# Kernel optimization log

Measured on AMD Instinct MI355X. Metric: run time of the kernel, lower is better.

The kernel has to match this reference:

```python
import jax, jax.numpy as jnp
import numpy as np

NCH, P, T, BS = 129, 4, 64000, 8
FRM_RATE, TC, HAIR_TC, SHFT, FAC = 16, 8.0, 0.5, 0, 1.0
L_FRM = FRM_RATE * (2 ** (4 + SHFT))            # 256 samples per frame
ALPHA = float(np.exp(-1.0 / (TC * 2 ** (4 + SHFT))))       # temporal integrator pole
BETA = float(np.exp(-1.0 / (HAIR_TC * 2 ** (4 + SHFT))))   # hair-cell LPF pole


def setup_inputs() -> dict:
    rng = np.random.default_rng(0)
    # stable order-4 cochlear IIRs: 2 conjugate pole pairs inside unit circle
    r = rng.uniform(0.8, 0.97, (NCH, P // 2))
    th = rng.uniform(0.05, np.pi - 0.05, (NCH, P // 2))
    A = np.stack([
        np.poly(np.concatenate([r[c] * np.exp(1j * th[c]), r[c] * np.exp(-1j * th[c])])).real
        for c in range(NCH)
    ]).astype(np.float32)                        # [NCH, P+1], A[:,0]==1
    B = (rng.standard_normal((NCH, P + 1)) * 0.1).astype(np.float32)
    key = jax.random.key(0)
    wav = jax.random.normal(key, (BS, T), dtype=jnp.float32)
    return {"wavData": wav, "coch_B": jnp.asarray(B), "coch_A": jnp.asarray(A)}


def iir_lfilter(b, a, x):
    # b, a: [nCh, P+1] (a[:,0] == 1), x: [bs, T] -> y: [nCh, bs, T]
    # direct-form II transposed, all channels in one scan over time
    bt = b[:, None, :]                           # [nCh, 1, P+1]
    at = a[:, None, :]
    z0 = jnp.zeros((b.shape[0], x.shape[0], b.shape[1] - 1), x.dtype)

    def step(z, xt):                             # z: [nCh, bs, P], xt: [bs]
        y = bt[..., 0] * xt[None, :] + z[..., 0]
        z_shift = jnp.concatenate([z[..., 1:], jnp.zeros_like(z[..., :1])], -1)
        z = z_shift + bt[..., 1:] * xt[None, :, None] - at[..., 1:] * y[..., None]
        return z, y

    _, y = jax.lax.scan(step, z0, x.T)           # y: [T, nCh, bs]
    return jnp.moveaxis(y, 0, -1)                # [nCh, bs, T]


def first_order_iir(x, c):
    # y[t] = x[t] + c * y[t-1] along the last axis (lfilter b=[1,0], a=[1,-c])
    def combine(e1, e2):
        a1, b1 = e1
        a2, b2 = e2
        return a1 * a2, b1 * a2 + b2

    coef = jnp.full_like(x, jnp.asarray(c, x.dtype))
    _, y = jax.lax.associative_scan(combine, (coef, x), axis=-1)
    return y


def reference(wavData, coch_B, coch_A):
    y1 = iir_lfilter(coch_B, coch_A, wavData)        # cochlear filterbank [nCh, bs, T]
    y2 = jax.nn.sigmoid(FAC * y1)                    # hair-cell nonlinearity
    y2 = first_order_iir(y2, BETA)                   # hair-cell membrane LPF
    y2_prev = jnp.concatenate([y2[:1], y2[:-1]], 0)  # previous channel (ch 0 diffs itself -> 0)
    y4 = jnp.maximum(y2 - y2_prev, 0.0)              # lateral inhibition + half-wave rectify
    y5 = first_order_iir(y4, ALPHA)                  # temporal integration (alpha != 0 branch)
    aud = y5[..., 0:T - 1:L_FRM]                     # frame-rate downsample [nCh, bs, nFrm]
    return jnp.transpose(aud, (1, 0, 2))             # [bs, nCh, nFrm]
```

## Files before the change

### kernel.cpp

```cpp
#include <hip/hip_runtime.h>
#include <math.h>

#define NCH 129
#define BS 8
#define TLEN 64000
#define CHUNK 256
#define WARM 64
#define NH 250
#define TILE 256
#define LFRM 256
#define NFRM 250
#define NSEQ (NCH * BS)
#define NBK (BS * NFRM)
#define NT (BS * NH)
#define KA_EDGE 16
#define KC_EDGE 8
#define KC_MAIN (NBK / 4)
#define SEG 25
#define LSEG 10
#define SGRP 17

#define SEQ4(h, b, c) ((size_t)(h) * NSEQ + (size_t)(b) * NCH + (c))

typedef float f2 __attribute__((ext_vector_type(2)));

__device__ __forceinline__ f2 mk2(float a, float b) { f2 r; r.x = a; r.y = b; return r; }

__device__ __forceinline__ f2 fma2(f2 a, f2 b, f2 c) {
#if __has_builtin(__builtin_elementwise_fma)
    return __builtin_elementwise_fma(a, b, c);
#else
    f2 r; r.x = fmaf(a.x, b.x, c.x); r.y = fmaf(a.y, b.y, c.y); return r;
#endif
}

__device__ __forceinline__ f2 sig2(f2 v) {
    f2 r;
    r.x = __builtin_amdgcn_rcpf(1.0f + __expf(-v.x));
    r.y = __builtin_amdgcn_rcpf(1.0f + __expf(-v.y));
    return r;
}

struct C2 { f2 b0, b1, b2, b3, b4, a1, a2, a3, a4; };

__device__ __forceinline__ C2 load_coef2(const float* __restrict__ B,
                                         const float* __restrict__ A,
                                         int cx, int cy) {
    C2 q;
    q.b0 = mk2(B[cx * 5 + 0], B[cy * 5 + 0]);
    q.b1 = mk2(B[cx * 5 + 1], B[cy * 5 + 1]);
    q.b2 = mk2(B[cx * 5 + 2], B[cy * 5 + 2]);
    q.b3 = mk2(B[cx * 5 + 3], B[cy * 5 + 3]);
    q.b4 = mk2(B[cx * 5 + 4], B[cy * 5 + 4]);
    q.a1 = mk2(A[cx * 5 + 1], A[cy * 5 + 1]);
    q.a2 = mk2(A[cx * 5 + 2], A[cy * 5 + 2]);
    q.a3 = mk2(A[cx * 5 + 3], A[cy * 5 + 3]);
    q.a4 = mk2(A[cx * 5 + 4], A[cy * 5 + 4]);
    return q;
}

__device__ __forceinline__ f2 iir2_step(const C2& q, float x,
                                        f2& z0, f2& z1, f2& z2, f2& z3) {
    f2 xx = mk2(x, x);
    f2 y = fma2(q.b0, xx, z0);
    z0 = fma2(-q.a1, y, fma2(q.b1, xx, z1));
    z1 = fma2(-q.a2, y, fma2(q.b2, xx, z2));
    z2 = fma2(-q.a3, y, fma2(q.b3, xx, z3));
    z3 = fma2(-q.a4, y, q.b4 * xx);
    return y;
}

struct Coef { float b0, b1, b2, b3, b4, a1, a2, a3, a4; };
__device__ __forceinline__ Coef load_coef(const float* __restrict__ B,
                                          const float* __restrict__ A, int c) {
    Coef q;
    q.b0 = B[c * 5 + 0]; q.b1 = B[c * 5 + 1]; q.b2 = B[c * 5 + 2];
    q.b3 = B[c * 5 + 3]; q.b4 = B[c * 5 + 4];
    q.a1 = A[c * 5 + 1]; q.a2 = A[c * 5 + 2];
    q.a3 = A[c * 5 + 3]; q.a4 = A[c * 5 + 4];
    return q;
}
__device__ __forceinline__ float iir_step(const Coef& q, float x,
                                          float& z0, float& z1, float& z2, float& z3) {
    float y = fmaf(q.b0, x, z0);
    z0 = fmaf(-q.a1, y, fmaf(q.b1, x, z1));
    z1 = fmaf(-q.a2, y, fmaf(q.b2, x, z2));
    z2 = fmaf(-q.a3, y, fmaf(q.b3, x, z3));
    z3 = fmaf(-q.a4, y, q.b4 * x);
    return y;
}

#define WSTEP(xv)                                                              \
    { f2 y_ = iir2_step(q, (xv), z0, z1, z2, z3);                              \
      u = fma2(beta2, u, sig2(y_)); }
#define MSTEP(xv)                                                              \
    { f2 y_ = iir2_step(q, (xv), z0, z1, z2, z3);                              \
      u = fma2(beta2, u, sig2(y_));                                            \
      float un_ = __shfl_down(u.x, 1, 64);                                     \
      float y4o_ = fmaxf(u.y - u.x, 0.0f);                                     \
      float y4e_ = fmaxf(pend_un - pend_ub, 0.0f);                             \
      g2 = fma2(alpha2, g2, mk2(y4o_, y4e_));                                  \
      pend_un = un_; pend_ub = u.y; }

#define MDECL(X) float X##00, X##01, X##02, X##03, X##10, X##11, X##12, X##13, \
                       X##20, X##21, X##22, X##23, X##30, X##31, X##32, X##33
#define MCOPY(D, S) D##00=S##00; D##01=S##01; D##02=S##02; D##03=S##03;        \
                    D##10=S##10; D##11=S##11; D##12=S##12; D##13=S##13;        \
                    D##20=S##20; D##21=S##21; D##22=S##22; D##23=S##23;        \
                    D##30=S##30; D##31=S##31; D##32=S##32; D##33=S##33
#define MROW(R, X, Y, i)                                                       \
    R##i##0 = fmaf(X##i##0, Y##00, fmaf(X##i##1, Y##10, fmaf(X##i##2, Y##20, X##i##3 * Y##30))); \
    R##i##1 = fmaf(X##i##0, Y##01, fmaf(X##i##1, Y##11, fmaf(X##i##2, Y##21, X##i##3 * Y##31))); \
    R##i##2 = fmaf(X##i##0, Y##02, fmaf(X##i##1, Y##12, fmaf(X##i##2, Y##22, X##i##3 * Y##32))); \
    R##i##3 = fmaf(X##i##0, Y##03, fmaf(X##i##1, Y##13, fmaf(X##i##2, Y##23, X##i##3 * Y##33)))
#define MMUL(R, X, Y) MROW(R, X, Y, 0); MROW(R, X, Y, 1); MROW(R, X, Y, 2); MROW(R, X, Y, 3)
#define MV(r, X, v)                                                            \
    r.x = fmaf(X##00, v.x, fmaf(X##01, v.y, fmaf(X##02, v.z, X##03 * v.w)));   \
    r.y = fmaf(X##10, v.x, fmaf(X##11, v.y, fmaf(X##12, v.z, X##13 * v.w)));   \
    r.z = fmaf(X##20, v.x, fmaf(X##21, v.y, fmaf(X##22, v.z, X##23 * v.w)));   \
    r.w = fmaf(X##30, v.x, fmaf(X##31, v.y, fmaf(X##32, v.z, X##33 * v.w)))
#define BUILD_MPOW(M1, a1, a2, a3, a4, NSQ)                                    \
    M1##00 = -(a1); M1##01 = 1.f; M1##02 = 0.f; M1##03 = 0.f;                  \
    M1##10 = -(a2); M1##11 = 0.f; M1##12 = 1.f; M1##13 = 0.f;                  \
    M1##20 = -(a3); M1##21 = 0.f; M1##22 = 0.f; M1##23 = 1.f;                  \
    M1##30 = -(a4); M1##31 = 0.f; M1##32 = 0.f; M1##33 = 0.f;                  \
    for (int s_ = 0; s_ < (NSQ); ++s_) { MDECL(T_); MMUL(T_, M1, M1); MCOPY(M1, T_); }

#define AFF_STEP(M, e, d)                                                      \
    {   float4 t_; MV(t_, M, e);                                               \
        e.x = t_.x + d.x; e.y = t_.y + d.y;                                    \
        e.z = t_.z + d.z; e.w = t_.w + d.w; }

__global__ __launch_bounds__(128, 8) void kA_forced_state(
        const float* __restrict__ wav, const float* __restrict__ B,
        const float* __restrict__ A, float* __restrict__ D,
        float* __restrict__ W) {
    __shared__ float xs[CHUNK];
    int blk = blockIdx.x;
    if (blk < KA_EDGE) {
        int item = blk * 128 + threadIdx.x;
        if (item >= NT) return;
        int b = item / NH;
        int h = item - b * NH;
        const float* xg = wav + (size_t)b * TLEN + (size_t)h * CHUNK;
        Coef q = load_coef(B, A, 128);
        float z0 = 0.f, z1 = 0.f, z2 = 0.f, z3 = 0.f;
        #pragma unroll 4
        for (int j = 0; j < CHUNK - WARM; ++j) {
            (void)iir_step(q, xg[j], z0, z1, z2, z3);
        }
        ((float4*)W)[SEQ4(h, b, 128)] = make_float4(z0, z1, z2, z3);
        #pragma unroll 4
        for (int j = CHUNK - WARM; j < CHUNK; ++j) {
            (void)iir_step(q, xg[j], z0, z1, z2, z3);
        }
        ((float4*)D)[SEQ4(h, b, 128)] = make_float4(z0, z1, z2, z3);
        return;
    }
    int mblk = blk - KA_EDGE;
    int b = mblk / NH;
    int h = mblk - b * NH;
    const float* xg = wav + (size_t)b * TLEN + (size_t)h * CHUNK;
    xs[threadIdx.x] = xg[threadIdx.x];
    xs[threadIdx.x + 128] = xg[threadIdx.x + 128];
    __syncthreads();
    int c = threadIdx.x;
    Coef q = load_coef(B, A, c);
    float z0 = 0.f, z1 = 0.f, z2 = 0.f, z3 = 0.f;
    #pragma unroll 8
    for (int j = 0; j < CHUNK - WARM; ++j) {
        (void)iir_step(q, xs[j], z0, z1, z2, z3);
    }
    ((float4*)W)[SEQ4(h, b, c)] = make_float4(z0, z1, z2, z3);
    #pragma unroll 8
    for (int j = CHUNK - WARM; j < CHUNK; ++j) {
        (void)iir_step(q, xs[j], z0, z1, z2, z3);
    }
    ((float4*)D)[SEQ4(h, b, c)] = make_float4(z0, z1, z2, z3);
}

__global__ __launch_bounds__(64) void kB1_fold(
        const float* __restrict__ A, const float* __restrict__ D,
        float* __restrict__ E) {
    int seg = blockIdx.x / SGRP;
    int s = (blockIdx.x % SGRP) * 64 + threadIdx.x;
    if (s >= NSEQ) return;
    int c = s % NCH;
    float a1 = A[c * 5 + 1], a2 = A[c * 5 + 2], a3 = A[c * 5 + 3], a4 = A[c * 5 + 4];
    MDECL(M1); BUILD_MPOW(M1, a1, a2, a3, a4, 8);
    const float4* db = (const float4*)D;
    float4 e = make_float4(0.f, 0.f, 0.f, 0.f);
    size_t base = (size_t)seg * LSEG * NSEQ + s;
    #pragma unroll
    for (int i = 0; i < LSEG; ++i) {
        float4 d = db[base + (size_t)i * NSEQ];
        AFF_STEP(M1, e, d);
    }
    ((float4*)E)[(size_t)seg * NSEQ + s] = e;
}

__global__ __launch_bounds__(64) void kB2_carry(
        const float* __restrict__ A, float* __restrict__ E) {
    int s = blockIdx.x * 64 + threadIdx.x;
    if (s >= NSEQ) return;
    int c = s % NCH;
    float a1 = A[c * 5 + 1], a2 = A[c * 5 + 2], a3 = A[c * 5 + 3], a4 = A[c * 5 + 4];
    MDECL(M1); BUILD_MPOW(M1, a1, a2, a3, a4, 8);
    MDECL(P2); MMUL(P2, M1, M1);
    MDECL(P4); MMUL(P4, P2, P2);
    MDECL(P8); MMUL(P8, P4, P4);
    MDECL(ML); MMUL(ML, P8, P2);
    float4* E4 = (float4*)E;
    float4 Z = make_float4(0.f, 0.f, 0.f, 0.f);
    float4 Eseg = E4[s];
    for (int seg = 0; seg < SEG; ++seg) {
        float4 Enext;
        if (seg + 1 < SEG) Enext = E4[(size_t)(seg + 1) * NSEQ + s];
        else               Enext = Z;
        E4[(size_t)seg * NSEQ + s] = Z;
        AFF_STEP(ML, Z, Eseg);
        Eseg = Enext;
    }
}

__global__ __launch_bounds__(64) void kB3_replay(
        const float* __restrict__ A, const float* __restrict__ D,
        const float* __restrict__ W, float* __restrict__ ZW,
        const float* __restrict__ E) {
    int seg = blockIdx.x / SGRP;
    int s = (blockIdx.x % SGRP) * 64 + threadIdx.x;
    if (s >= NSEQ) return;
    int c = s % NCH;
    float a1 = A[c * 5 + 1], a2 = A[c * 5 + 2], a3 = A[c * 5 + 3], a4 = A[c * 5 + 4];
    MDECL(M64); BUILD_MPOW(M64, a1, a2, a3, a4, 6);
    MDECL(M128); MMUL(M128, M64, M64);
    MDECL(M192); MMUL(M192, M128, M64);
    MDECL(M256); MMUL(M256, M128, M128);
    const float4* db = (const float4*)D;
    const float4* wb = (const float4*)W;
    float4* zwb = (float4*)ZW;
    float4 z = ((const float4*)E)[(size_t)seg * NSEQ + s];
    int h0 = seg * LSEG;
    #pragma unroll
    for (int i = 0; i < LSEG; ++i) {
        size_t ix = (size_t)(h0 + i) * NSEQ + s;
        float4 d = db[ix];
        float4 w = wb[ix];
        float4 zw; MV(zw, M192, z);
        zw.x += w.x; zw.y += w.y; zw.z += w.z; zw.w += w.w;
        zwb[ix] = zw;
        AFF_STEP(M256, z, d);
    }
}

__global__ __launch_bounds__(256, 8) void kC_main(
        const float* __restrict__ wav, const float* __restrict__ B,
        const float* __restrict__ A, const float* __restrict__ ZW,
        float* __restrict__ G, float* __restrict__ y4f,
        float beta, float alpha) {
    __shared__ float4 xs4[4 * 80];
    int blk = blockIdx.x;
    const f2 beta2 = mk2(beta, beta);
    const f2 alpha2 = mk2(alpha, alpha);

    if (blk < KC_EDGE) {
        int item = blk * 256 + threadIdx.x;
        if (item >= NBK) return;
        int b = item / NFRM;
        int r = item - b * NFRM;
        C2 q = load_coef2(B, A, 127, 128);
        f2 z0 = mk2(0.f, 0.f), z1 = z0, z2 = z0, z3 = z0, u = z0;
        const float* xg;
        if (r > 0) {
            float4 vx = ((const float4*)ZW)[SEQ4(r - 1, b, 127)];
            float4 vy = ((const float4*)ZW)[SEQ4(r - 1, b, 128)];
            z0 = mk2(vx.x, vy.x); z1 = mk2(vx.y, vy.y);
            z2 = mk2(vx.z, vy.z); z3 = mk2(vx.w, vy.w);
            xg = wav + (size_t)b * TLEN + (size_t)r * TILE - WARM;
            #pragma unroll 2
            for (int j = 0; j < WARM; ++j) WSTEP(xg[j]);
            xg += WARM;
        } else {
            xg = wav + (size_t)b * TLEN;
        }
        float g4 = 0.f, yfirst = 0.f;
        #pragma unroll 2
        for (int j = 0; j < TILE; ++j) {
            f2 y_ = iir2_step(q, xg[j], z0, z1, z2, z3);
            u = fma2(beta2, u, sig2(y_));
            float y4 = fmaxf(u.y - u.x, 0.0f);
            if (j == 0) yfirst = y4;
            g4 = fmaf(alpha, g4, y4);
        }
        size_t idx = ((size_t)b * NFRM + r) * NCH + 128;
        G[idx] = g4;
        y4f[idx] = yfirst;
        return;
    }

    int wave = threadIdx.x >> 6;
    int t = threadIdx.x & 63;
    int tile = (blk - KC_EDGE) * 4 + wave;
    int b = tile / NFRM;
    int r = tile - b * NFRM;
    int n4 = (r > 0) ? 80 : 64;
    const float* xg = wav + (size_t)b * TLEN +
                      ((r > 0) ? (size_t)r * TILE - WARM : (size_t)0);
    float4* seg = xs4 + wave * 80;
    for (int i = t; i < n4; i += 64) seg[i] = ((const float4*)xg)[i];
    __syncthreads();

    int cA = 2 * t, cB = 2 * t + 1;
    C2 q = load_coef2(B, A, cA, cB);
    f2 z0 = mk2(0.f, 0.f), z1 = z0, z2 = z0, z3 = z0, u = z0;
    int gbase = 0;
    if (r > 0) {
        float4 vx = ((const float4*)ZW)[SEQ4(r - 1, b, cA)];
        float4 vy = ((const float4*)ZW)[SEQ4(r - 1, b, cB)];
        z0 = mk2(vx.x, vy.x); z1 = mk2(vx.y, vy.y);
        z2 = mk2(vx.z, vy.z); z3 = mk2(vx.w, vy.w);
        for (int g = 0; g < WARM / 4; ++g) {
            float4 xq = seg[g];
            WSTEP(xq.x); WSTEP(xq.y); WSTEP(xq.z); WSTEP(xq.w);
        }
        gbase = WARM / 4;
    }

    f2 g2;
    float fo, fe, pend_un, pend_ub;
    {
        float4 xq = seg[gbase];
        f2 y_ = iir2_step(q, xq.x, z0, z1, z2, z3);
        u = fma2(beta2, u, sig2(y_));
        float un_ = __shfl_down(u.x, 1, 64);
        float y4o_ = fmaxf(u.y - u.x, 0.0f);
        fo = y4o_;
        g2 = mk2(y4o_, 0.0f);
        pend_un = un_; pend_ub = u.y;
        y_ = iir2_step(q, xq.y, z0, z1, z2, z3);
        u = fma2(beta2, u, sig2(y_));
        un_ = __shfl_down(u.x, 1, 64);
        y4o_ = fmaxf(u.y - u.x, 0.0f);
        float y4e_ = fmaxf(pend_un - pend_ub, 0.0f);
        fe = y4e_;
        g2 = fma2(alpha2, g2, mk2(y4o_, y4e_));
        pend_un = un_; pend_ub = u.y;
        MSTEP(xq.z); MSTEP(xq.w);
    }
    for (int g = gbase + 1; g < gbase + TILE / 4; ++g) {
        float4 xq = seg[g];
        MSTEP(xq.x); MSTEP(xq.y); MSTEP(xq.z); MSTEP(xq.w);
    }
    float y4e_last = fmaxf(pend_un - pend_ub, 0.0f);
    float go = g2.x;
    float ge = fmaf(alpha, g2.y, y4e_last);

    size_t base = ((size_t)b * NFRM + r) * NCH;
    G[base + cB] = go;
    y4f[base + cB] = fo;
    if (t < 63) {
        G[base + cB + 1] = ge;
        y4f[base + cB + 1] = fe;
    }
}

#define KD_LOAD(gn, yn, i)                                                     \
    {   int kk = k0 + (i); int kcl = (kk < NFRM) ? kk : (NFRM - 1);            \
        size_t ix = ((size_t)b * NFRM + kcl) * NCH + c;                        \
        gn = G[ix]; yn = y4f[ix];                                              \
        if (kk >= NFRM) { gn = 0.f; yn = 0.f; } }
#define KD_REPLAY(gn, yn, i)                                                   \
    {   int kk = k0 + (i);                                                     \
        if (kk < NFRM) o[kk] = fmaf(alpha, sv, yn);                            \
        sv = fmaf(aL, sv, gn); }

__global__ __launch_bounds__(256) void kD_scan_par(
        const float* __restrict__ G, const float* __restrict__ y4f,
        float* __restrict__ out, float alpha, float aL) {
    int id = blockIdx.x * 4 + (threadIdx.x >> 6);
    int lane = threadIdx.x & 63;
    if (id >= NSEQ) return;
    int b = id / NCH;
    int c = id - b * NCH;
    float* o = out + (size_t)id * NFRM;
    int k0 = lane * 4;
    if (c == 0) {
        #pragma unroll
        for (int i = 0; i < 4; ++i) {
            int kk = k0 + i;
            if (kk < NFRM) o[kk] = 0.0f;
        }
        return;
    }
    float g0, g1, g2v, g3, y0, y1, y2v, y3;
    KD_LOAD(g0, y0, 0); KD_LOAD(g1, y1, 1); KD_LOAD(g2v, y2v, 2); KD_LOAD(g3, y3, 3);
    float e = g0;
    e = fmaf(aL, e, g1);
    e = fmaf(aL, e, g2v);
    e = fmaf(aL, e, g3);
    float aL2 = aL * aL;
    float f = aL2 * aL2;
    for (int s = 0; s < 6; ++s) {
        int off = 1 << s;
        float src = __shfl_up(e, off, 64);
        if (lane < off) src = 0.f;
        e = fmaf(f, src, e);
        f = f * f;
    }
    float sv = __shfl_up(e, 1, 64);
    if (lane == 0) sv = 0.f;
    KD_REPLAY(g0, y0, 0); KD_REPLAY(g1, y1, 1);
    KD_REPLAY(g2v, y2v, 2); KD_REPLAY(g3, y3, 3);
}

extern "C" void kernel_launch(void* const* d_in, const int* in_sizes, int n_in,
                              void* d_out, int out_size, void* d_ws, size_t ws_size,
                              hipStream_t stream) {
    const float* wav = (const float*)d_in[0];
    const float* Bc  = (const float*)d_in[1];
    const float* Ac  = (const float*)d_in[2];
    float* out = (float*)d_out;

    float* D   = (float*)d_ws;
    float* W   = D + (size_t)NH * NSEQ * 4;
    float* ZW  = W + (size_t)NH * NSEQ * 4;
    float* G   = ZW + (size_t)NH * NSEQ * 4;
    float* y4f = G + (size_t)NBK * NCH;
    float* E   = y4f + (size_t)NBK * NCH;

    const float alpha  = (float)exp(-1.0 / 128.0);
    const float beta   = (float)exp(-1.0 / 8.0);
    const float alphaL = (float)exp(-256.0 / 128.0);

    kA_forced_state<<<KA_EDGE + NT, 128, 0, stream>>>(wav, Bc, Ac, D, W);
    kB1_fold<<<SEG * SGRP, 64, 0, stream>>>(Ac, D, E);
    kB2_carry<<<SGRP, 64, 0, stream>>>(Ac, E);
    kB3_replay<<<SEG * SGRP, 64, 0, stream>>>(Ac, D, W, ZW, E);
    kC_main<<<KC_EDGE + KC_MAIN, 256, 0, stream>>>(wav, Bc, Ac, ZW, G, y4f, beta, alpha);
    kD_scan_par<<<NSEQ / 4, 256, 0, stream>>>(G, y4f, out, alpha, alphaL);
}
```

Before: 132.6 us.

## Pack two channels per thread in forced-state kernel with packed FMA

The forced-state kernel now runs one 64-lane wave per time tile, with each lane handling two channels through packed v_pk_fma_f32 via inline asm. The block grows to 256 threads covering four tiles, and each wave loads its input into LDS as float4. Negated A coefficients are precomputed so the packed FMAs need no negation, which also affects the other users of iir2_step. The aim is to halve the per-channel instruction count and widen blocks, at the cost of fewer threads in flight and inline asm that blocks compiler scheduling.

```diff
diff --git a/kernel.cpp b/kernel.cpp
--- a/kernel.cpp
+++ b/kernel.cpp
@@ -13,7 +13,8 @@
 #define NSEQ (NCH * BS)
 #define NBK (BS * NFRM)
 #define NT (BS * NH)
-#define KA_EDGE 16
+#define KA_EDGE 8
+#define KA_MAIN (NT / 4)
 #define KC_EDGE 8
 #define KC_MAIN (NBK / 4)
 #define SEG 25
@@ -27,11 +28,14 @@
 __device__ __forceinline__ f2 mk2(float a, float b) { f2 r; r.x = a; r.y = b; return r; }
 
 __device__ __forceinline__ f2 fma2(f2 a, f2 b, f2 c) {
-#if __has_builtin(__builtin_elementwise_fma)
-    return __builtin_elementwise_fma(a, b, c);
-#else
-    f2 r; r.x = fmaf(a.x, b.x, c.x); r.y = fmaf(a.y, b.y, c.y); return r;
-#endif
+    f2 d;
+    asm("v_pk_fma_f32 %0, %1, %2, %3" : "=v"(d) : "v"(a), "v"(b), "v"(c));
+    return d;
+}
+__device__ __forceinline__ f2 mul2(f2 a, f2 b) {
+    f2 d;
+    asm("v_pk_mul_f32 %0, %1, %2" : "=v"(d) : "v"(a), "v"(b));
+    return d;
 }
 
 __device__ __forceinline__ f2 sig2(f2 v) {
@@ -41,7 +45,7 @@
     return r;
 }
 
-struct C2 { f2 b0, b1, b2, b3, b4, a1, a2, a3, a4; };
+struct C2 { f2 b0, b1, b2, b3, b4, na1, na2, na3, na4; };
 
 __device__ __forceinline__ C2 load_coef2(const float* __restrict__ B,
                                          const float* __restrict__ A,
@@ -52,10 +56,10 @@
     q.b2 = mk2(B[cx * 5 + 2], B[cy * 5 + 2]);
     q.b3 = mk2(B[cx * 5 + 3], B[cy * 5 + 3]);
     q.b4 = mk2(B[cx * 5 + 4], B[cy * 5 + 4]);
-    q.a1 = mk2(A[cx * 5 + 1], A[cy * 5 + 1]);
-    q.a2 = mk2(A[cx * 5 + 2], A[cy * 5 + 2]);
-    q.a3 = mk2(A[cx * 5 + 3], A[cy * 5 + 3]);
-    q.a4 = mk2(A[cx * 5 + 4], A[cy * 5 + 4]);
+    q.na1 = mk2(-A[cx * 5 + 1], -A[cy * 5 + 1]);
+    q.na2 = mk2(-A[cx * 5 + 2], -A[cy * 5 + 2]);
+    q.na3 = mk2(-A[cx * 5 + 3], -A[cy * 5 + 3]);
+    q.na4 = mk2(-A[cx * 5 + 4], -A[cy * 5 + 4]);
     return q;
 }
 
@@ -63,10 +67,10 @@
                                         f2& z0, f2& z1, f2& z2, f2& z3) {
     f2 xx = mk2(x, x);
     f2 y = fma2(q.b0, xx, z0);
-    z0 = fma2(-q.a1, y, fma2(q.b1, xx, z1));
-    z1 = fma2(-q.a2, y, fma2(q.b2, xx, z2));
-    z2 = fma2(-q.a3, y, fma2(q.b3, xx, z3));
-    z3 = fma2(-q.a4, y, q.b4 * xx);
+    z0 = fma2(q.na1, y, fma2(q.b1, xx, z1));
+    z1 = fma2(q.na2, y, fma2(q.b2, xx, z2));
+    z2 = fma2(q.na3, y, fma2(q.b3, xx, z3));
+    z3 = fma2(q.na4, y, mul2(q.b4, xx));
     return y;
 }
 
@@ -90,6 +94,7 @@
     return y;
 }
 
+#define ISTEP(xv) { (void)iir2_step(q, (xv), z0, z1, z2, z3); }
 #define WSTEP(xv)                                                              \
     { f2 y_ = iir2_step(q, (xv), z0, z1, z2, z3);                              \
       u = fma2(beta2, u, sig2(y_)); }
@@ -131,14 +136,14 @@
         e.x = t_.x + d.x; e.y = t_.y + d.y;                                    \
         e.z = t_.z + d.z; e.w = t_.w + d.w; }
 
-__global__ __launch_bounds__(128, 8) void kA_forced_state(
+__global__ __launch_bounds__(256, 8) void kA_forced_state(
         const float* __restrict__ wav, const float* __restrict__ B,
         const float* __restrict__ A, float* __restrict__ D,
         float* __restrict__ W) {
-    __shared__ float xs[CHUNK];
+    __shared__ float4 xs4[4 * 64];
     int blk = blockIdx.x;
     if (blk < KA_EDGE) {
-        int item = blk * 128 + threadIdx.x;
+        int item = blk * 256 + threadIdx.x;
         if (item >= NT) return;
         int b = item / NH;
         int h = item - b * NH;
@@ -157,26 +162,31 @@
         ((float4*)D)[SEQ4(h, b, 128)] = make_float4(z0, z1, z2, z3);
         return;
     }
-    int mblk = blk - KA_EDGE;
-    int b = mblk / NH;
-    int h = mblk - b * NH;
+    int wave = threadIdx.x >> 6;
+    int t = threadIdx.x & 63;
+    int tile = (blk - KA_EDGE) * 4 + wave;
+    int b = tile / NH;
+    int h = tile - b * NH;
     const float* xg = wav + (size_t)b * TLEN + (size_t)h * CHUNK;
-    xs[threadIdx.x] = xg[threadIdx.x];
-    xs[threadIdx.x + 128] = xg[threadIdx.x + 128];
+    float4* seg = xs4 + wave * 64;
+    seg[t] = ((const float4*)xg)[t];
     __syncthreads();
-    int c = threadIdx.x;
-    Coef q = load_coef(B, A, c);
-    float z0 = 0.f, z1 = 0.f, z2 = 0.f, z3 = 0.f;
-    #pragma unroll 8
-    for (int j = 0; j < CHUNK - WARM; ++j) {
-        (void)iir_step(q, xs[j], z0, z1, z2, z3);
-    }
-    ((float4*)W)[SEQ4(h, b, c)] = make_float4(z0, z1, z2, z3);
-    #pragma unroll 8
-    for (int j = CHUNK - WARM; j < CHUNK; ++j) {
-        (void)iir_step(q, xs[j], z0, z1, z2, z3);
-    }
-    ((float4*)D)[SEQ4(h, b, c)] = make_float4(z0, z1, z2, z3);
+
+    int cA = 2 * t, cB = 2 * t + 1;
+    C2 q = load_coef2(B, A, cA, cB);
+    f2 z0 = mk2(0.f, 0.f), z1 = z0, z2 = z0, z3 = z0;
+    for (int g = 0; g < (CHUNK - WARM) / 4; ++g) {
+        float4 xq = seg[g];
+        ISTEP(xq.x); ISTEP(xq.y); ISTEP(xq.z); ISTEP(xq.w);
+    }
+    ((float4*)W)[SEQ4(h, b, cA)] = make_float4(z0.x, z1.x, z2.x, z3.x);
+    ((float4*)W)[SEQ4(h, b, cB)] = make_float4(z0.y, z1.y, z2.y, z3.y);
+    for (int g = (CHUNK - WARM) / 4; g < CHUNK / 4; ++g) {
+        float4 xq = seg[g];
+        ISTEP(xq.x); ISTEP(xq.y); ISTEP(xq.z); ISTEP(xq.w);
+    }
+    ((float4*)D)[SEQ4(h, b, cA)] = make_float4(z0.x, z1.x, z2.x, z3.x);
+    ((float4*)D)[SEQ4(h, b, cB)] = make_float4(z0.y, z1.y, z2.y, z3.y);
 }
 
 __global__ __launch_bounds__(64) void kB1_fold(
@@ -432,7 +442,7 @@
     const float beta   = (float)exp(-1.0 / 8.0);
     const float alphaL = (float)exp(-256.0 / 128.0);
 
-    kA_forced_state<<<KA_EDGE + NT, 128, 0, stream>>>(wav, Bc, Ac, D, W);
+    kA_forced_state<<<KA_EDGE + KA_MAIN, 256, 0, stream>>>(wav, Bc, Ac, D, W);
     kB1_fold<<<SEG * SGRP, 64, 0, stream>>>(Ac, D, E);
     kB2_carry<<<SGRP, 64, 0, stream>>>(Ac, E);
     kB3_replay<<<SEG * SGRP, 64, 0, stream>>>(Ac, D, W, ZW, E);
```

New measurement: 131.6 us. Within noise of the previous version (-0.7%).

## Remap main kernels to one channel per lane with split channel halves

Applied to the files above, without the earlier changes.

The main path of kC now gives each lane a single channel. Channels 0-63 and 64-127 run in separate waves, replacing the old scheme where each lane handled two adjacent channels with packed float2 math. Lateral inhibition uses a scalar shfl_up. The wave boundary pairs (63,64) and (127,128) move to edge blocks. kA is regrouped into 256-thread blocks that each cover two tiles and load input with float4. The change roughly doubles the lane count and shortens each lane's dependent chain, at the cost of losing packed-FMA throughput and adding extra edge work.

```diff
diff --git a/kernel.cpp b/kernel.cpp
--- a/kernel.cpp
+++ b/kernel.cpp
@@ -8,14 +8,14 @@
 #define WARM 64
 #define NH 250
 #define TILE 256
-#define LFRM 256
 #define NFRM 250
 #define NSEQ (NCH * BS)
 #define NBK (BS * NFRM)
 #define NT (BS * NH)
-#define KA_EDGE 16
-#define KC_EDGE 8
-#define KC_MAIN (NBK / 4)
+#define KA_EDGE 8
+#define KA_MAIN (NT / 2)
+#define KC_EDGE 16
+#define KC_MAIN (NBK / 2)
 #define SEG 25
 #define LSEG 10
 #define SGRP 17
@@ -34,11 +34,11 @@
 #endif
 }
 
+__device__ __forceinline__ float sigf(float v) {
+    return __builtin_amdgcn_rcpf(1.0f + __expf(-v));
+}
 __device__ __forceinline__ f2 sig2(f2 v) {
-    f2 r;
-    r.x = __builtin_amdgcn_rcpf(1.0f + __expf(-v.x));
-    r.y = __builtin_amdgcn_rcpf(1.0f + __expf(-v.y));
-    return r;
+    f2 r; r.x = sigf(v.x); r.y = sigf(v.y); return r;
 }
 
 struct C2 { f2 b0, b1, b2, b3, b4, a1, a2, a3, a4; };
@@ -90,17 +90,20 @@
     return y;
 }
 
+#define SISTEP(xv) { (void)iir_step(q, (xv), z0, z1, z2, z3); }
+#define SWSTEP(xv)                                                             \
+    { float y_ = iir_step(q, (xv), z0, z1, z2, z3);                            \
+      u = fmaf(beta, u, sigf(y_)); }
+#define SSTEP(xv)                                                              \
+    { float y_ = iir_step(q, (xv), z0, z1, z2, z3);                            \
+      u = fmaf(beta, u, sigf(y_));                                             \
+      float un_ = __shfl_up(u, 1, 64);                                         \
+      float y4_ = fmaxf(u - un_, 0.0f);                                        \
+      gacc = fmaf(alpha, gacc, y4_); }
+
 #define WSTEP(xv)                                                              \
     { f2 y_ = iir2_step(q, (xv), z0, z1, z2, z3);                              \
       u = fma2(beta2, u, sig2(y_)); }
-#define MSTEP(xv)                                                              \
-    { f2 y_ = iir2_step(q, (xv), z0, z1, z2, z3);                              \
-      u = fma2(beta2, u, sig2(y_));                                            \
-      float un_ = __shfl_down(u.x, 1, 64);                                     \
-      float y4o_ = fmaxf(u.y - u.x, 0.0f);                                     \
-      float y4e_ = fmaxf(pend_un - pend_ub, 0.0f);                             \
-      g2 = fma2(alpha2, g2, mk2(y4o_, y4e_));                                  \
-      pend_un = un_; pend_ub = u.y; }
 
 #define MDECL(X) float X##00, X##01, X##02, X##03, X##10, X##11, X##12, X##13, \
                        X##20, X##21, X##22, X##23, X##30, X##31, X##32, X##33
@@ -131,14 +134,14 @@
         e.x = t_.x + d.x; e.y = t_.y + d.y;                                    \
         e.z = t_.z + d.z; e.w = t_.w + d.w; }
 
-__global__ __launch_bounds__(128, 8) void kA_forced_state(
+__global__ __launch_bounds__(256, 8) void kA_forced_state(
         const float* __restrict__ wav, const float* __restrict__ B,
         const float* __restrict__ A, float* __restrict__ D,
         float* __restrict__ W) {
-    __shared__ float xs[CHUNK];
+    __shared__ float4 xs4[2 * 64];
     int blk = blockIdx.x;
     if (blk < KA_EDGE) {
-        int item = blk * 128 + threadIdx.x;
+        int item = blk * 256 + threadIdx.x;
         if (item >= NT) return;
         int b = item / NH;
         int h = item - b * NH;
@@ -157,24 +160,30 @@
         ((float4*)D)[SEQ4(h, b, 128)] = make_float4(z0, z1, z2, z3);
         return;
     }
-    int mblk = blk - KA_EDGE;
-    int b = mblk / NH;
-    int h = mblk - b * NH;
+    int wave = threadIdx.x >> 6;
+    int t = threadIdx.x & 63;
+    int pair = wave >> 1;
+    int half = wave & 1;
+    int pt = threadIdx.x & 127;
+    int tile = (blk - KA_EDGE) * 2 + pair;
+    int b = tile / NH;
+    int h = tile - b * NH;
     const float* xg = wav + (size_t)b * TLEN + (size_t)h * CHUNK;
-    xs[threadIdx.x] = xg[threadIdx.x];
-    xs[threadIdx.x + 128] = xg[threadIdx.x + 128];
+    float4* seg = xs4 + pair * 64;
+    if (pt < 64) seg[pt] = ((const float4*)xg)[pt];
     __syncthreads();
-    int c = threadIdx.x;
+
+    int c = (half ? 64 : 0) + t;
     Coef q = load_coef(B, A, c);
     float z0 = 0.f, z1 = 0.f, z2 = 0.f, z3 = 0.f;
-    #pragma unroll 8
-    for (int j = 0; j < CHUNK - WARM; ++j) {
-        (void)iir_step(q, xs[j], z0, z1, z2, z3);
+    for (int g = 0; g < (CHUNK - WARM) / 4; ++g) {
+        float4 xq = seg[g];
+        SISTEP(xq.x); SISTEP(xq.y); SISTEP(xq.z); SISTEP(xq.w);
     }
     ((float4*)W)[SEQ4(h, b, c)] = make_float4(z0, z1, z2, z3);
-    #pragma unroll 8
-    for (int j = CHUNK - WARM; j < CHUNK; ++j) {
-        (void)iir_step(q, xs[j], z0, z1, z2, z3);
+    for (int g = (CHUNK - WARM) / 4; g < CHUNK / 4; ++g) {
+        float4 xq = seg[g];
+        SISTEP(xq.x); SISTEP(xq.y); SISTEP(xq.z); SISTEP(xq.w);
     }
     ((float4*)D)[SEQ4(h, b, c)] = make_float4(z0, z1, z2, z3);
 }
@@ -258,22 +267,25 @@
         const float* __restrict__ A, const float* __restrict__ ZW,
         float* __restrict__ G, float* __restrict__ y4f,
         float beta, float alpha) {
-    __shared__ float4 xs4[4 * 80];
+    __shared__ float4 xs4[2 * 80];
     int blk = blockIdx.x;
-    const f2 beta2 = mk2(beta, beta);
-    const f2 alpha2 = mk2(alpha, alpha);
 
     if (blk < KC_EDGE) {
+        const f2 beta2 = mk2(beta, beta);
         int item = blk * 256 + threadIdx.x;
-        if (item >= NBK) return;
-        int b = item / NFRM;
-        int r = item - b * NFRM;
-        C2 q = load_coef2(B, A, 127, 128);
+        if (item >= 2 * NBK) return;
+        int sel = item / NBK;
+        int it2 = item - sel * NBK;
+        int b = it2 / NFRM;
+        int r = it2 - b * NFRM;
+        int cx = sel ? 63 : 127;
+        int cy = sel ? 64 : 128;
+        C2 q = load_coef2(B, A, cx, cy);
         f2 z0 = mk2(0.f, 0.f), z1 = z0, z2 = z0, z3 = z0, u = z0;
         const float* xg;
         if (r > 0) {
-            float4 vx = ((const float4*)ZW)[SEQ4(r - 1, b, 127)];
-            float4 vy = ((const float4*)ZW)[SEQ4(r - 1, b, 128)];
+            float4 vx = ((const float4*)ZW)[SEQ4(r - 1, b, cx)];
+            float4 vy = ((const float4*)ZW)[SEQ4(r - 1, b, cy)];
             z0 = mk2(vx.x, vy.x); z1 = mk2(vx.y, vy.y);
             z2 = mk2(vx.z, vy.z); z3 = mk2(vx.w, vy.w);
             xg = wav + (size_t)b * TLEN + (size_t)r * TILE - WARM;
@@ -292,7 +304,7 @@
             if (j == 0) yfirst = y4;
             g4 = fmaf(alpha, g4, y4);
         }
-        size_t idx = ((size_t)b * NFRM + r) * NCH + 128;
+        size_t idx = ((size_t)b * NFRM + r) * NCH + cy;
         G[idx] = g4;
         y4f[idx] = yfirst;
         return;
@@ -300,67 +312,52 @@
 
     int wave = threadIdx.x >> 6;
     int t = threadIdx.x & 63;
-    int tile = (blk - KC_EDGE) * 4 + wave;
+    int pair = wave >> 1;
+    int half = wave & 1;
+    int pt = threadIdx.x & 127;
+    int tile = (blk - KC_EDGE) * 2 + pair;
     int b = tile / NFRM;
     int r = tile - b * NFRM;
     int n4 = (r > 0) ? 80 : 64;
     const float* xg = wav + (size_t)b * TLEN +
                       ((r > 0) ? (size_t)r * TILE - WARM : (size_t)0);
-    float4* seg = xs4 + wave * 80;
-    for (int i = t; i < n4; i += 64) seg[i] = ((const float4*)xg)[i];
+    float4* seg = xs4 + pair * 80;
+    if (pt < n4) seg[pt] = ((const float4*)xg)[pt];
     __syncthreads();
 
-    int cA = 2 * t, cB = 2 * t + 1;
-    C2 q = load_coef2(B, A, cA, cB);
-    f2 z0 = mk2(0.f, 0.f), z1 = z0, z2 = z0, z3 = z0, u = z0;
+    int c = (half ? 64 : 0) + t;
+    Coef q = load_coef(B, A, c);
+    float z0 = 0.f, z1 = 0.f, z2 = 0.f, z3 = 0.f, u = 0.f;
     int gbase = 0;
     if (r > 0) {
-        float4 vx = ((const float4*)ZW)[SEQ4(r - 1, b, cA)];
-        float4 vy = ((const float4*)ZW)[SEQ4(r - 1, b, cB)];
-        z0 = mk2(vx.x, vy.x); z1 = mk2(vx.y, vy.y);
-        z2 = mk2(vx.z, vy.z); z3 = mk2(vx.w, vy.w);
+        float4 v = ((const float4*)ZW)[SEQ4(r - 1, b, c)];
+        z0 = v.x; z1 = v.y; z2 = v.z; z3 = v.w;
         for (int g = 0; g < WARM / 4; ++g) {
             float4 xq = seg[g];
-            WSTEP(xq.x); WSTEP(xq.y); WSTEP(xq.z); WSTEP(xq.w);
+            SWSTEP(xq.x); SWSTEP(xq.y); SWSTEP(xq.z); SWSTEP(xq.w);
         }
         gbase = WARM / 4;
     }
 
-    f2 g2;
-    float fo, fe, pend_un, pend_ub;
+    float gacc, yfirst;
     {
         float4 xq = seg[gbase];
-        f2 y_ = iir2_step(q, xq.x, z0, z1, z2, z3);
-        u = fma2(beta2, u, sig2(y_));
-        float un_ = __shfl_down(u.x, 1, 64);
-        float y4o_ = fmaxf(u.y - u.x, 0.0f);
-        fo = y4o_;
-        g2 = mk2(y4o_, 0.0f);
-        pend_un = un_; pend_ub = u.y;
-        y_ = iir2_step(q, xq.y, z0, z1, z2, z3);
-        u = fma2(beta2, u, sig2(y_));
-        un_ = __shfl_down(u.x, 1, 64);
-        y4o_ = fmaxf(u.y - u.x, 0.0f);
-        float y4e_ = fmaxf(pend_un - pend_ub, 0.0f);
-        fe = y4e_;
-        g2 = fma2(alpha2, g2, mk2(y4o_, y4e_));
-        pend_un = un_; pend_ub = u.y;
-        MSTEP(xq.z); MSTEP(xq.w);
+        float y_ = iir_step(q, xq.x, z0, z1, z2, z3);
+        u = fmaf(beta, u, sigf(y_));
+        float un_ = __shfl_up(u, 1, 64);
+        yfirst = fmaxf(u - un_, 0.0f);
+        gacc = yfirst;
+        SSTEP(xq.y); SSTEP(xq.z); SSTEP(xq.w);
     }
     for (int g = gbase + 1; g < gbase + TILE / 4; ++g) {
         float4 xq = seg[g];
-        MSTEP(xq.x); MSTEP(xq.y); MSTEP(xq.z); MSTEP(xq.w);
-    }
-    float y4e_last = fmaxf(pend_un - pend_ub, 0.0f);
-    float go = g2.x;
-    float ge = fmaf(alpha, g2.y, y4e_last);
-
-    size_t base = ((size_t)b * NFRM + r) * NCH;
-    G[base + cB] = go;
-    y4f[base + cB] = fo;
-    if (t < 63) {
-        G[base + cB + 1] = ge;
-        y4f[base + cB + 1] = fe;
+        SSTEP(xq.x); SSTEP(xq.y); SSTEP(xq.z); SSTEP(xq.w);
+    }
+
+    if (half == 0 || t > 0) {
+        size_t base = ((size_t)b * NFRM + r) * NCH;
+        G[base + c] = gacc;
+        y4f[base + c] = yfirst;
     }
 }
 
@@ -432,7 +429,7 @@
     const float beta   = (float)exp(-1.0 / 8.0);
     const float alphaL = (float)exp(-256.0 / 128.0);
 
-    kA_forced_state<<<KA_EDGE + NT, 128, 0, stream>>>(wav, Bc, Ac, D, W);
+    kA_forced_state<<<KA_EDGE + KA_MAIN, 256, 0, stream>>>(wav, Bc, Ac, D, W);
     kB1_fold<<<SEG * SGRP, 64, 0, stream>>>(Ac, D, E);
     kB2_carry<<<SGRP, 64, 0, stream>>>(Ac, E);
     kB3_replay<<<SEG * SGRP, 64, 0, stream>>>(Ac, D, W, ZW, E);
```

Result: slower. 143.8 us (+8.5%).
